# Performance work log

Hardware: AMD Instinct MI355X
Metric: run time of the kernel (lower is better)

The kernel has to match this reference:

```python
import jax, jax.numpy as jnp
import numpy as np

B, T, N, C_IN, C_OUT, D_E, GH, H = 16, 12, 2048, 64, 64, 16, 32, 4


def setup_inputs() -> dict:
    key = jax.random.key(0)
    ks = jax.random.split(key, 12)
    f = jax.random.normal
    return {
        "x": f(ks[0], (B, T, N, C_IN), jnp.float32),
        "init_state": jnp.zeros((B, N, C_OUT), jnp.float32),
        "node_embeddings": f(ks[1], (N, D_E), jnp.float32),
        "gat_W": f(ks[2], (H, D_E, GH), jnp.float32) * 0.3,
        "gat_a_src": f(ks[3], (H, GH), jnp.float32) * 0.3,
        "gat_a_dst": f(ks[4], (H, GH), jnp.float32) * 0.3,
        "wp_gates": f(ks[5], (D_E, 2, C_IN + C_OUT, 2 * C_OUT), jnp.float32) * 0.05,
        "bp_gates": f(ks[6], (D_E, 2 * C_OUT), jnp.float32) * 0.05,
        "wp_cand": f(ks[7], (D_E, 2, C_IN + C_OUT, C_OUT), jnp.float32) * 0.05,
        "bp_cand": f(ks[8], (D_E, C_OUT), jnp.float32) * 0.05,
        "tc_w": f(ks[9], (C_OUT, C_OUT, 1, 3), jnp.float32) * 0.05,
        "tc_b": jnp.zeros((C_OUT,), jnp.float32),
        "rc_w": f(ks[10], (C_OUT, C_IN, 1, 1), jnp.float32) * 0.05,
        "rc_b": jnp.zeros((C_OUT,), jnp.float32),
        "ln_g": jnp.ones((C_OUT,), jnp.float32),
        "ln_b": jnp.zeros((C_OUT,), jnp.float32),
    }


def _forward(x, init_state, node_embeddings, gat_W, gat_a_src, gat_a_dst,
             wp_gates, bp_gates, wp_cand, bp_cand, tc_w, tc_b, rc_w, rc_b, ln_g, ln_b):
    E = node_embeddings
    # GAT-style adaptive support over node embeddings: [N, N]
    h = jnp.einsum('nd,hdf->hnf', E, gat_W)                       # [H,N,GH]
    s = jnp.einsum('hnf,hf->hn', h, gat_a_src)
    d = jnp.einsum('hnf,hf->hn', h, gat_a_dst)
    e = jax.nn.leaky_relu(s[:, :, None] + d[:, None, :], 0.2)     # [H,N,N]
    A = jax.nn.softmax(e, axis=-1).mean(0)                        # [N,N]
    # node-adaptive weights (NAL): per-node weights from embedding pools
    W_g = jnp.einsum('nd,dkio->nkio', E, wp_gates)                # [N,2,Cin+Cout,2Cout]
    b_g = E @ bp_gates                                            # [N,2Cout]
    W_c = jnp.einsum('nd,dkio->nkio', E, wp_cand)
    b_c = E @ bp_cand

    def gconv(inp, W, b):
        # cheb order-2 supports [I, A] over inp: [B,N,C] -> [B,N,out]
        xg = jnp.stack([inp, jnp.einsum('mn,bnc->bmc', A, inp)], 2)
        return jnp.einsum('bnki,nkio->bno', xg, W) + b

    def step(state, xt):
        zr = jax.nn.sigmoid(gconv(jnp.concatenate([xt, state], -1), W_g, b_g))
        z, r = jnp.split(zr, 2, axis=-1)
        hc = jnp.tanh(gconv(jnp.concatenate([xt, r * state], -1), W_c, b_c))
        new = z * state + (1.0 - z) * hc
        return new, new

    last, inner = jax.lax.scan(step, init_state, jnp.swapaxes(x, 0, 1))
    inner = jnp.swapaxes(inner, 0, 1)                             # [B,T,N,C]

    cur = jnp.transpose(inner, (0, 3, 2, 1))                      # [B,C,N,T]
    tco = jax.lax.conv_general_dilated(
        cur, tc_w, (1, 1), [(0, 0), (1, 1)],
        dimension_numbers=('NCHW', 'OIHW', 'NCHW')) + tc_b[None, :, None, None]
    xp = jnp.transpose(x, (0, 3, 2, 1))                           # [B,Cin,N,T]
    res = jnp.einsum('oc,bcnt->bont', rc_w[:, :, 0, 0], xp) + rc_b[None, :, None, None]
    y = jnp.transpose(jax.nn.relu(res + tco), (0, 3, 2, 1))       # [B,T,N,C]
    mu = y.mean(-1, keepdims=True)
    var = y.var(-1, keepdims=True)
    y = (y - mu) / jnp.sqrt(var + 1e-5) * ln_g + ln_b
    return y, last


def reference(x, init_state, node_embeddings, gat_W, gat_a_src, gat_a_dst,
              wp_gates, bp_gates, wp_cand, bp_cand, tc_w, tc_b, rc_w, rc_b, ln_g, ln_b):
    y, last = _forward(x, init_state, node_embeddings, gat_W, gat_a_src, gat_a_dst,
                       wp_gates, bp_gates, wp_cand, bp_cand, tc_w, tc_b, rc_w, rc_b, ln_g, ln_b)
    return (y, last)
```

## Files before the change

### kernel.cpp

```cpp
#include <hip/hip_runtime.h>
#include <stdint.h>

#define B_  16
#define T_  12
#define N_  2048
#define DE_ 16
#define GH_ 32
#define NH_ 4

typedef __attribute__((ext_vector_type(8)))  short short8;
typedef __attribute__((ext_vector_type(4)))  float f32x4;
typedef __attribute__((ext_vector_type(16))) float f32x16;

__device__ __forceinline__ unsigned short f2b(float f){
  unsigned u = __float_as_uint(f);
  return (unsigned short)((u + 0x7fffu + ((u>>16)&1u)) >> 16);
}
__device__ __forceinline__ float b2f(unsigned short h){
  return __uint_as_float(((unsigned)h)<<16);
}
__device__ __forceinline__ unsigned pk2(float a, float b){
  return (unsigned)f2b(a) | ((unsigned)f2b(b)<<16);
}
__device__ __forceinline__ float lrelu(float v){ return v>=0.f ? v : 0.2f*v; }

__device__ __forceinline__ void gl16(const void* g, void* l){
  __builtin_amdgcn_global_load_lds((const __attribute__((address_space(1))) void*)g,
                                   (__attribute__((address_space(3))) void*)l, 16, 0, 0);
}

__global__ __launch_bounds__(256) void k_gat_sd(const float* __restrict__ E, const float* __restrict__ gW,
    const float* __restrict__ asrc, const float* __restrict__ adst,
    float* __restrict__ sArr, float* __restrict__ dArr)
{
  int id = blockIdx.x*256 + threadIdx.x;
  int h = id >> 11, n = id & 2047;
  float hv[GH_];
#pragma unroll
  for (int f=0; f<GH_; ++f) hv[f]=0.f;
  for (int d=0; d<DE_; ++d){
    float e = E[n*DE_+d];
    const float* wr = gW + (h*DE_+d)*GH_;
#pragma unroll
    for (int f=0; f<GH_; ++f) hv[f] += e*wr[f];
  }
  float s=0.f, dd=0.f;
#pragma unroll
  for (int f=0; f<GH_; ++f){ s += hv[f]*asrc[h*GH_+f]; dd += hv[f]*adst[h*GH_+f]; }
  sArr[h*N_+n]=s; dArr[h*N_+n]=dd;
}

__global__ __launch_bounds__(256) void k_dmax(const float* __restrict__ dArr, float* __restrict__ dmax){
  __shared__ float red[256];
  int h = blockIdx.x, t = threadIdx.x;
  float m = -1e30f;
  for (int i=t;i<N_;i+=256) m = fmaxf(m, dArr[h*N_+i]);
  red[t]=m; __syncthreads();
  for (int s=128;s>0;s>>=1){ if (t<s) red[t]=fmaxf(red[t],red[t+s]); __syncthreads(); }
  if (t==0) dmax[h]=red[0];
}

__global__ __launch_bounds__(256) void k_denom(const float* __restrict__ sArr, const float* __restrict__ dArr,
                                               const float* __restrict__ dmax, float* __restrict__ denom){
  __shared__ float red[256];
  int m = blockIdx.x, h = blockIdx.y, t = threadIdx.x;
  float sm = sArr[h*N_+m];
  float shift = lrelu(sm + dmax[h]);
  float acc=0.f;
  for (int i=t;i<N_;i+=256) acc += __expf(lrelu(sm + dArr[h*N_+i]) - shift);
  red[t]=acc; __syncthreads();
  for (int s=128;s>0;s>>=1){ if (t<s) red[t]+=red[t+s]; __syncthreads(); }
  if (t==0) denom[h*N_+m]=red[0];
}

__global__ __launch_bounds__(256) void k_adj(const float* __restrict__ sArr, const float* __restrict__ dArr,
                                             const float* __restrict__ dmax, const float* __restrict__ denom,
                                             unsigned short* __restrict__ Abf){
  int m = blockIdx.x, t = threadIdx.x;
  float sm[NH_], sh[NH_], inv[NH_];
#pragma unroll
  for (int h=0;h<NH_;++h){ sm[h]=sArr[h*N_+m]; sh[h]=lrelu(sm[h]+dmax[h]); inv[h]=1.f/denom[h*N_+m]; }
  for (int n=t;n<N_;n+=256){
    float acc=0.f;
#pragma unroll
    for (int h=0;h<NH_;++h) acc += __expf(lrelu(sm[h]+dArr[h*N_+n]) - sh[h]) * inv[h];
    Abf[(long)m*N_+n] = f2b(acc*0.25f);
  }
}

__global__ __launch_bounds__(256) void k_xsw(const float* __restrict__ x,
                                             unsigned short* __restrict__ xsw)
{
  __shared__ unsigned short sT[256*64];
  int kb = blockIdx.x;
  int btB = blockIdx.y;
  int tid = threadIdx.x;
  int btl = tid>>6, kin = tid&63;
  int n  = kb*64 + kin;
  int bt = btB*4 + btl;
  const float* src = x + ((long)bt*N_ + n)*64;
  unsigned short row[64];
#pragma unroll
  for (int c4=0; c4<16; ++c4){
    float4 v = *(const float4*)(src + c4*4);
    row[c4*4+0]=f2b(v.x); row[c4*4+1]=f2b(v.y); row[c4*4+2]=f2b(v.z); row[c4*4+3]=f2b(v.w);
  }
  int g0 = kin>>3, e = kin&7;
#pragma unroll
  for (int c=0; c<64; ++c){
    int jl = btl*64 + c;
    int s = g0 ^ (c&7);
    sT[jl*64 + s*8 + e] = row[c];
  }
  __syncthreads();
  unsigned short* dst = xsw + ((long)kb*12288 + btB*256)*64;
  const uint4* sp = (const uint4*)sT;
  uint4* dp = (uint4*)dst;
  for (int i=tid; i<2048; i+=256) dp[i] = sp[i];
}

__global__ __launch_bounds__(256) void k_nalw(const float* __restrict__ E, const float* __restrict__ wp,
                                              unsigned short* __restrict__ Wout, int Osz){
  __shared__ float sS[256][17];
  __shared__ float sE[512*16];
  int o = blockIdx.x, q = blockIdx.y, t = threadIdx.x;
  int slot = t>>3, j = t&7;
  int kio = (((slot ^ (o&7))&31)<<3) | j;
  long dstride = 256L*Osz;
  for (int d=0; d<DE_; ++d) sS[t][d] = wp[d*dstride + (long)kio*Osz + o];
  for (int i=t; i<512*16; i+=256) sE[i] = E[q*512*16 + i];
  __syncthreads();
  unsigned short* out = Wout + (long)(q*512)*dstride + o*256 + t;
  for (int nn=0; nn<512; ++nn){
    float acc=0.f;
    const float* e = &sE[nn*16];
#pragma unroll
    for (int d=0; d<DE_; ++d) acc += e[d]*sS[t][d];
    out[(long)nn*dstride] = f2b(acc);
  }
}

__global__ __launch_bounds__(256) void k_nalb(const float* __restrict__ E, const float* __restrict__ bpg,
                                              const float* __restrict__ bpc,
                                              unsigned short* __restrict__ bg, unsigned short* __restrict__ bc){
  int id = blockIdx.x*256+threadIdx.x;
  int n = id/192, oo = id%192;
  float acc=0.f;
  if (oo<128){
    for (int d=0;d<DE_;++d) acc += E[n*DE_+d]*bpg[d*128+oo];
    bg[n*128+oo]=f2b(acc);
  } else {
    int c=oo-128;
    for (int d=0;d<DE_;++d) acc += E[n*DE_+d]*bpc[d*64+c];
    bc[n*64+c]=f2b(acc);
  }
}

__global__ __launch_bounds__(256) void k_wcat(const float* __restrict__ tcw, const float* __restrict__ rcw,
                                              unsigned short* __restrict__ Wcat){
  int id = blockIdx.x*256+threadIdx.x;
  int o = id>>8, k = id&255;
  float v;
  if (k<192){ int dt=k>>6, c=k&63; v = tcw[(o*64+c)*3+dt]; }
  else v = rcw[o*64 + (k&63)];
  int pos = o*256 + ((((k>>3)&31) ^ (o&7))<<3) + (k&7);
  Wcat[pos] = f2b(v);
}

__global__ __launch_bounds__(256) void k_init2(const float* __restrict__ init, float* __restrict__ st,
                                               unsigned short* __restrict__ stb){
  int i = blockIdx.x*256+threadIdx.x;
  float v = init[i]; st[i]=v;
  int c = i&63, n = (i>>6)&2047, b = i>>17;
  int kb = n>>6, kin = n&63;
  int j = b*64 + c;
  int s = (kin>>3) ^ (c&7);
  stb[((long)kb*1024 + j)*64 + s*8 + (kin&7)] = f2b(v);
}

template<int BM, int BN, int JTOT>
__global__ __launch_bounds__(256) void k_gemm2(
    const unsigned short* __restrict__ A,
    const unsigned short* __restrict__ Bs,
    unsigned short* __restrict__ D)
{
  constexpr int MBLK = 2048/BM, MPX = MBLK/8;
  constexpr int NIA = BM*64*2/(256*16);
  constexpr int NIB = BN*64*2/(256*16);
  constexpr int WTM = BM/2, WTN = BN/2;
  constexpr int MTC = WTM/32, NTC = WTN/32;
  __shared__ __align__(16) unsigned short sA[BM*64];
  __shared__ __align__(16) unsigned short sB[BN*64];
  int bid = blockIdx.x;
  int xcd = bid & 7, idx = bid >> 3;
  int mB = xcd*MPX + (idx % MPX);
  int jB = idx / MPX;
  int tid = threadIdx.x, w = tid>>6, l = tid&63;
  int wm = w&1, wn = w>>1;
  f32x16 acc[MTC][NTC];
#pragma unroll
  for (int a=0;a<MTC;++a)
#pragma unroll
    for (int b=0;b<NTC;++b)
#pragma unroll
      for (int i=0;i<16;++i) acc[a][b][i]=0.f;

  for (int kb=0; kb<32; ++kb){
    __syncthreads();
#pragma unroll
    for (int i=0;i<NIA;++i){
      int c = (w*NIA+i)*64 + l;
      int row = c>>3, slot = c&7, g = slot ^ (row&7);
      gl16((const char*)A + (((long)(mB*BM+row))*2048 + kb*64 + g*8)*2,
           (char*)sA + (w*NIA+i)*1024);
    }
    const char* bt = (const char*)(Bs + ((long)kb*JTOT + jB*BN)*64);
#pragma unroll
    for (int i=0;i<NIB;++i)
      gl16(bt + ((w*NIB+i)*64 + l)*16, (char*)sB + (w*NIB+i)*1024);
    __syncthreads();
#pragma unroll
    for (int ks=0; ks<4; ++ks){
      int gk = ks*2 + (l>>5);
      short8 af[MTC];
#pragma unroll
      for (int mt=0; mt<MTC; ++mt){
        int row = wm*WTM + mt*32 + (l&31);
        af[mt] = *(const short8*)((const char*)sA + row*128 + ((gk ^ (row&7))<<4));
      }
#pragma unroll
      for (int nt=0; nt<NTC; ++nt){
        int jj = wn*WTN + nt*32 + (l&31);
        short8 bfv = *(const short8*)((const char*)sB + jj*128 + ((gk ^ (jj&7))<<4));
#pragma unroll
        for (int mt=0; mt<MTC; ++mt)
          acc[mt][nt] = __builtin_amdgcn_mfma_f32_32x32x16_bf16(af[mt], bfv, acc[mt][nt], 0,0,0);
      }
    }
  }
#pragma unroll
  for (int mt=0; mt<MTC; ++mt)
#pragma unroll
    for (int nt=0; nt<NTC; ++nt)
#pragma unroll
      for (int rg=0; rg<16; ++rg){
        int rl = wm*WTM + mt*32 + (rg&3) + 8*(rg>>2) + 4*(l>>5);
        int col = jB*BN + wn*WTN + nt*32 + (l&31);
        long m = (long)mB*BM + rl;
        D[m*JTOT + col] = f2b(acc[mt][nt][rg]);
      }
}

__global__ __launch_bounds__(256) void k_gates(
    const float* __restrict__ x, const float* __restrict__ st,
    const unsigned short* __restrict__ AXn, const unsigned short* __restrict__ AS,
    const unsigned short* __restrict__ Wg, const unsigned short* __restrict__ bg,
    float* __restrict__ zbuf, unsigned short* __restrict__ rsp,
    unsigned short* __restrict__ rsb, int t)
{
  __shared__ __align__(16) unsigned short sW[64*256];
  __shared__ __align__(16) unsigned short sX[16*256];
  int n = blockIdx.x, half = blockIdx.y;
  int tid = threadIdx.x, w = tid>>6, l = tid&63;
  const unsigned short* Wsrc = Wg + (long)n*32768 + half*16384;
#pragma unroll
  for (int i=0;i<8;++i){
    int c = (w*8+i)*64 + l;
    gl16((const char*)Wsrc + c*16, (char*)sW + (w*8+i)*1024);
  }
  int b = tid>>4, c16 = tid&15;
  uint4 g0, g1;
  if (c16 < 8){
    const float* p = (c16<4) ? (x  + (((long)(b*T_+t)*N_ + n)*64 + c16*16))
                             : (st + (((long)b*N_ + n)*64 + (c16-4)*16));
    float4 f0 = *(const float4*)(p+0), f1 = *(const float4*)(p+4);
    float4 f2v = *(const float4*)(p+8), f3 = *(const float4*)(p+12);
    g0.x = pk2(f0.x,f0.y); g0.y = pk2(f0.z,f0.w); g0.z = pk2(f1.x,f1.y); g0.w = pk2(f1.z,f1.w);
    g1.x = pk2(f2v.x,f2v.y); g1.y = pk2(f2v.z,f2v.w); g1.z = pk2(f3.x,f3.y); g1.w = pk2(f3.z,f3.w);
  } else {
    const unsigned short* p = (c16<12)
      ? (AXn + ((long)n*12288 + (b*T_+t)*64 + (c16-8)*16))
      : (AS  + ((long)n*1024  + b*64       + (c16-12)*16));
    g0 = *(const uint4*)(p); g1 = *(const uint4*)(p+8);
  }
  {
    int gg = c16*2;
    *(uint4*)((char*)sX + b*512 + (((gg  ) ^ (b&7))<<4)) = g0;
    *(uint4*)((char*)sX + b*512 + (((gg+1) ^ (b&7))<<4)) = g1;
  }
  __syncthreads();
  f32x4 acc;
#pragma unroll
  for (int i=0;i<4;++i) acc[i]=0.f;
  int orow = w*16 + (l&15);
  int arow = l&15;
#pragma unroll
  for (int ks=0; ks<8; ++ks){
    int g = ks*4 + (l>>4);
    short8 a = *(const short8*)((const char*)sX + arow*512 + ((g ^ (arow&7))<<4));
    short8 bb = *(const short8*)((const char*)sW + orow*512 + ((g ^ (orow&7))<<4));
    acc = __builtin_amdgcn_mfma_f32_16x16x32_bf16(a, bb, acc, 0,0,0);
  }
  int o = half*64 + orow;
  float bia = b2f(bg[n*128 + o]);
  int kb = n>>6, kin = n&63;
  int sw = (kin>>3) ^ (orow&7);
#pragma unroll
  for (int i=0;i<4;++i){
    int b2 = (l>>4)*4 + i;
    float v = acc[i] + bia;
    float sg = 1.f/(1.f+__expf(-v));
    long idx = ((long)b2*N_ + n)*64;
    if (half==0) zbuf[idx + o] = sg;
    else {
      float s0v = st[idx + orow];
      unsigned short rv = f2b(sg*s0v);
      rsp[idx + orow] = rv;
      rsb[((long)kb*1024 + b2*64 + orow)*64 + sw*8 + (kin&7)] = rv;
    }
  }
}

__global__ __launch_bounds__(256) void k_cand(
    const float* __restrict__ x, const float* __restrict__ zbuf,
    const unsigned short* __restrict__ AXn, const unsigned short* __restrict__ ARS,
    const unsigned short* __restrict__ rsp,
    const unsigned short* __restrict__ Wc, const unsigned short* __restrict__ bc,
    float* __restrict__ st, unsigned short* __restrict__ stb,
    unsigned short* __restrict__ inner, int t)
{
  __shared__ __align__(16) unsigned short sW[64*256];
  __shared__ __align__(16) unsigned short sX[16*256];
  int n = blockIdx.x;
  int tid = threadIdx.x, w = tid>>6, l = tid&63;
  const unsigned short* Wsrc = Wc + (long)n*16384;
#pragma unroll
  for (int i=0;i<8;++i){
    int c = (w*8+i)*64 + l;
    gl16((const char*)Wsrc + c*16, (char*)sW + (w*8+i)*1024);
  }
  int b = tid>>4, c16 = tid&15;
  uint4 g0, g1;
  if (c16 < 4){
    const float* p = x + (((long)(b*T_+t)*N_ + n)*64 + c16*16);
    float4 f0 = *(const float4*)(p+0), f1 = *(const float4*)(p+4);
    float4 f2v = *(const float4*)(p+8), f3 = *(const float4*)(p+12);
    g0.x = pk2(f0.x,f0.y); g0.y = pk2(f0.z,f0.w); g0.z = pk2(f1.x,f1.y); g0.w = pk2(f1.z,f1.w);
    g1.x = pk2(f2v.x,f2v.y); g1.y = pk2(f2v.z,f2v.w); g1.z = pk2(f3.x,f3.y); g1.w = pk2(f3.z,f3.w);
  } else {
    const unsigned short* p;
    if (c16<8)       p = rsp + (((long)b*N_ + n)*64 + (c16-4)*16);
    else if (c16<12) p = AXn + ((long)n*12288 + (b*T_+t)*64 + (c16-8)*16);
    else             p = ARS + ((long)n*1024  + b*64       + (c16-12)*16);
    g0 = *(const uint4*)(p); g1 = *(const uint4*)(p+8);
  }
  {
    int gg = c16*2;
    *(uint4*)((char*)sX + b*512 + (((gg  ) ^ (b&7))<<4)) = g0;
    *(uint4*)((char*)sX + b*512 + (((gg+1) ^ (b&7))<<4)) = g1;
  }
  __syncthreads();
  f32x4 acc;
#pragma unroll
  for (int i=0;i<4;++i) acc[i]=0.f;
  int orow = w*16 + (l&15);
  int arow = l&15;
#pragma unroll
  for (int ks=0; ks<8; ++ks){
    int g = ks*4 + (l>>4);
    short8 a = *(const short8*)((const char*)sX + arow*512 + ((g ^ (arow&7))<<4));
    short8 bb = *(const short8*)((const char*)sW + orow*512 + ((g ^ (orow&7))<<4));
    acc = __builtin_amdgcn_mfma_f32_16x16x32_bf16(a, bb, acc, 0,0,0);
  }
  float bia = b2f(bc[n*64 + orow]);
  int kb = n>>6, kin = n&63;
  int sw = (kin>>3) ^ (orow&7);
#pragma unroll
  for (int i=0;i<4;++i){
    int b2 = (l>>4)*4 + i;
    float hc = tanhf(acc[i] + bia);
    long idx = ((long)b2*N_ + n)*64 + orow;
    float zv = zbuf[idx];
    float olds = st[idx];
    float nv = zv*olds + (1.f-zv)*hc;
    st[idx]=nv;
    unsigned short nb = f2b(nv);
    stb[((long)kb*1024 + b2*64 + orow)*64 + sw*8 + (kin&7)] = nb;
    inner[((long)(b2*T_+t)*N_ + n)*64 + orow] = nb;
  }
}

__global__ __launch_bounds__(256) void k_post(
    const unsigned short* __restrict__ inner, const float* __restrict__ x,
    const unsigned short* __restrict__ Wcat,
    const float* __restrict__ tcb, const float* __restrict__ rcb,
    const float* __restrict__ lng, const float* __restrict__ lnb,
    float* __restrict__ out)
{
  __shared__ __align__(16) unsigned short sF[64*256];
  __shared__ __align__(16) unsigned short sW[64*256];
  int id = blockIdx.x;
  int bt = id>>5, nb = id&31;
  int b = bt/T_, t = bt%T_;
  int n0 = nb*64;
  int tid = threadIdx.x, w = tid>>6, l = tid&63;
#pragma unroll
  for (int i=0;i<8;++i){
    int c = (w*8+i)*64 + l;
    gl16((const char*)Wcat + c*16, (char*)sW + (w*8+i)*1024);
  }
  int row = tid&63, q = tid>>6;
  uint4 ch[8];
  if (q<3){
    int ts = t + q - 1;
    if (ts>=0 && ts<T_){
      const uint4* p = (const uint4*)(inner + (((long)(b*T_+ts)*N_) + n0+row)*64);
#pragma unroll
      for (int hh=0;hh<8;++hh) ch[hh]=p[hh];
    } else {
      uint4 zz; zz.x=0u; zz.y=0u; zz.z=0u; zz.w=0u;
#pragma unroll
      for (int hh=0;hh<8;++hh) ch[hh]=zz;
    }
  } else {
    const float4* p = (const float4*)(x + (((long)bt*N_) + n0+row)*64);
#pragma unroll
    for (int hh=0;hh<8;++hh){
      float4 u0=p[2*hh], u1=p[2*hh+1];
      ch[hh].x=pk2(u0.x,u0.y); ch[hh].y=pk2(u0.z,u0.w);
      ch[hh].z=pk2(u1.x,u1.y); ch[hh].w=pk2(u1.z,u1.w);
    }
  }
#pragma unroll
  for (int hh=0;hh<8;++hh){
    int g = q*8+hh;
    *(uint4*)((char*)sF + row*512 + ((g ^ (row&7))<<4)) = ch[hh];
  }
  __syncthreads();
  f32x4 acc[4];
#pragma unroll
  for (int ot=0; ot<4; ++ot)
#pragma unroll
    for (int i=0;i<4;++i) acc[ot][i]=0.f;
  int arow = w*16 + (l&15);
#pragma unroll
  for (int ks=0; ks<8; ++ks){
    int g = ks*4 + (l>>4);
    short8 a = *(const short8*)((const char*)sF + arow*512 + ((g ^ (arow&7))<<4));
#pragma unroll
    for (int ot=0; ot<4; ++ot){
      int o = ot*16 + (l&15);
      short8 bb = *(const short8*)((const char*)sW + o*512 + ((g ^ (o&7))<<4));
      acc[ot] = __builtin_amdgcn_mfma_f32_16x16x32_bf16(a, bb, acc[ot], 0,0,0);
    }
  }
  float s1[4]={0.f,0.f,0.f,0.f}, s2[4]={0.f,0.f,0.f,0.f};
#pragma unroll
  for (int ot=0; ot<4; ++ot){
    int o = ot*16 + (l&15);
    float bia = tcb[o] + rcb[o];
#pragma unroll
    for (int i=0;i<4;++i){
      float v = fmaxf(acc[ot][i] + bia, 0.f);
      acc[ot][i] = v;
      s1[i]+=v; s2[i]+=v*v;
    }
  }
#pragma unroll
  for (int msk=1; msk<16; msk<<=1){
#pragma unroll
    for (int i=0;i<4;++i){
      s1[i] += __shfl_xor(s1[i], msk, 64);
      s2[i] += __shfl_xor(s2[i], msk, 64);
    }
  }
#pragma unroll
  for (int i=0;i<4;++i){
    float mu = s1[i]*(1.f/64.f);
    float var = s2[i]*(1.f/64.f) - mu*mu;
    float rstd = rsqrtf(fmaxf(var,0.f)+1e-5f);
    int rr = n0 + w*16 + (l>>4)*4 + i;
#pragma unroll
    for (int ot=0; ot<4; ++ot){
      int o = ot*16 + (l&15);
      out[(((long)bt*N_) + rr)*64 + o] = (acc[ot][i]-mu)*rstd*lng[o] + lnb[o];
    }
  }
}

extern "C" void kernel_launch(void* const* d_in, const int* in_sizes, int n_in,
                              void* d_out, int out_size, void* d_ws, size_t ws_size,
                              hipStream_t stream)
{
  const float* x    = (const float*)d_in[0];
  const float* init = (const float*)d_in[1];
  const float* E    = (const float*)d_in[2];
  const float* gW   = (const float*)d_in[3];
  const float* asrc = (const float*)d_in[4];
  const float* adst = (const float*)d_in[5];
  const float* wpg  = (const float*)d_in[6];
  const float* bpg  = (const float*)d_in[7];
  const float* wpc  = (const float*)d_in[8];
  const float* bpc  = (const float*)d_in[9];
  const float* tcw  = (const float*)d_in[10];
  const float* tcb  = (const float*)d_in[11];
  const float* rcw  = (const float*)d_in[12];
  const float* rcb  = (const float*)d_in[13];
  const float* lng  = (const float*)d_in[14];
  const float* lnb  = (const float*)d_in[15];
  float* out = (float*)d_out;

  char* p = (char*)d_ws;
  auto alloc = [&](size_t bytes)->char*{ char* r = p; p += (bytes + 255) & ~(size_t)255; return r; };
  unsigned short* Abf  = (unsigned short*)alloc((size_t)N_*N_*2);
  unsigned short* Wg   = (unsigned short*)alloc((size_t)N_*32768*2);
  unsigned short* Wc   = (unsigned short*)alloc((size_t)N_*16384*2);
  unsigned short* bg   = (unsigned short*)alloc((size_t)N_*128*2);
  unsigned short* bc   = (unsigned short*)alloc((size_t)N_*64*2);
  unsigned short* xsw  = (unsigned short*)alloc((size_t)N_*12288*2);
  unsigned short* AXn  = (unsigned short*)alloc((size_t)N_*12288*2);
  unsigned short* AS   = (unsigned short*)alloc((size_t)N_*1024*2);
  unsigned short* ARS  = (unsigned short*)alloc((size_t)N_*1024*2);
  unsigned short* rsb  = (unsigned short*)alloc((size_t)N_*1024*2);
  unsigned short* rsp  = (unsigned short*)alloc((size_t)N_*1024*2);
  unsigned short* stb  = (unsigned short*)alloc((size_t)N_*1024*2);
  unsigned short* inner= (unsigned short*)alloc((size_t)B_*T_*N_*64*2);
  unsigned short* Wcat = (unsigned short*)alloc((size_t)64*256*2);
  float* sArr = (float*)alloc((size_t)NH_*N_*4);
  float* dArr = (float*)alloc((size_t)NH_*N_*4);
  float* dmax = (float*)alloc((size_t)NH_*4);
  float* denom= (float*)alloc((size_t)NH_*N_*4);
  float* stf  = (float*)alloc((size_t)B_*N_*64*4);
  float* zbuf = (float*)alloc((size_t)B_*N_*64*4);

  k_gat_sd<<<32,256,0,stream>>>(E,gW,asrc,adst,sArr,dArr);
  k_dmax<<<4,256,0,stream>>>(dArr,dmax);
  k_denom<<<dim3(N_,NH_),256,0,stream>>>(sArr,dArr,dmax,denom);
  k_adj<<<N_,256,0,stream>>>(sArr,dArr,dmax,denom,Abf);
  k_xsw<<<dim3(32,48),256,0,stream>>>(x,xsw);
  k_nalw<<<dim3(128,4),256,0,stream>>>(E,wpg,Wg,128);
  k_nalw<<<dim3(64,4),256,0,stream>>>(E,wpc,Wc,64);
  k_nalb<<<1536,256,0,stream>>>(E,bpg,bpc,bg,bc);
  k_wcat<<<64,256,0,stream>>>(tcw,rcw,Wcat);
  k_init2<<<(B_*N_*64)/256,256,0,stream>>>(init,stf,stb);

  k_gemm2<128,128,12288><<<1536,256,0,stream>>>(Abf, xsw, AXn);

  for (int t=0; t<T_; ++t){
    k_gemm2<64,64,1024><<<512,256,0,stream>>>(Abf, stb, AS);
    k_gates<<<dim3(N_,2),256,0,stream>>>(x,stf,AXn,AS,Wg,bg,zbuf,rsp,rsb,t);
    k_gemm2<64,64,1024><<<512,256,0,stream>>>(Abf, rsb, ARS);
    k_cand<<<N_,256,0,stream>>>(x,zbuf,AXn,ARS,rsp,Wc,bc,stf,stb,inner,t);
  }

  k_post<<<B_*T_*32,256,0,stream>>>(inner,x,Wcat,tcb,rcb,lng,lnb,out);
  hipMemcpyAsync(out + (size_t)B_*T_*N_*64, stf, (size_t)B_*N_*64*4,
                 hipMemcpyDeviceToDevice, stream);
}
```

Before: 2.102 ms.

## Precompute input-dependent gate/candidate terms for all timesteps before the recurrence

Splits the per-node weights into input (x, A·x) and state parts and computes the x-dependent contribution for all 12 timesteps in one batched MFMA kernel (k_pre) ahead of the scan. Inside the loop, the gates and candidate kernels then only load half the weights and do half the K dimension, adding the precomputed term from preA. The step loop also swaps the generic GEMM for a dedicated double-buffered 64x64 kernel with XCD-aware block mapping. This adds a large preA buffer (stored bf16, an extra rounding) and reuses workspace memory by aliasing buffers.

```diff
diff --git a/kernel.cpp b/kernel.cpp
--- a/kernel.cpp
+++ b/kernel.cpp
@@ -119,24 +119,30 @@
   for (int i=tid; i<2048; i+=256) dp[i] = sp[i];
 }
 
-__global__ __launch_bounds__(256) void k_nalw(const float* __restrict__ E, const float* __restrict__ wp,
-                                              unsigned short* __restrict__ Wout, int Osz){
-  __shared__ float sS[256][17];
+__global__ __launch_bounds__(256) void k_nalw2(const float* __restrict__ E, const float* __restrict__ src,
+                                               unsigned short* __restrict__ dst,
+                                               int Osrc, int kofs, int o_dst0, long strideN)
+{
   __shared__ float sE[512*16];
-  int o = blockIdx.x, q = blockIdx.y, t = threadIdx.x;
-  int slot = t>>3, j = t&7;
-  int kio = (((slot ^ (o&7))&31)<<3) | j;
-  long dstride = 256L*Osz;
-  for (int d=0; d<DE_; ++d) sS[t][d] = wp[d*dstride + (long)kio*Osz + o];
-  for (int i=t; i<512*16; i+=256) sE[i] = E[q*512*16 + i];
+  int or_ = blockIdx.x, q = blockIdx.y, t = threadIdx.x;
+  int pos = t & 127, nsub = t >> 7;
+  int s = pos >> 3, j = pos & 7;
+  int k = ((s ^ (or_&7)) << 3) | j;
+  int cheb = k >> 6, i = kofs + (k & 63);
+  float wreg[16];
+#pragma unroll
+  for (int d=0; d<DE_; ++d)
+    wreg[d] = src[(long)d*2*128*Osrc + (long)cheb*128*Osrc + (long)i*Osrc + or_];
+  for (int idx=t; idx<512*16; idx+=256) sE[idx] = E[q*512*16 + idx];
   __syncthreads();
-  unsigned short* out = Wout + (long)(q*512)*dstride + o*256 + t;
-  for (int nn=0; nn<512; ++nn){
+  unsigned short* out = dst + (long)(q*512)*strideN + (o_dst0 + or_)*128 + pos;
+  for (int nn=0; nn<256; ++nn){
+    int nl = nn*2 + nsub;
+    const float* e = &sE[nl*16];
     float acc=0.f;
-    const float* e = &sE[nn*16];
-#pragma unroll
-    for (int d=0; d<DE_; ++d) acc += e[d]*sS[t][d];
-    out[(long)nn*dstride] = f2b(acc);
+#pragma unroll
+    for (int d=0; d<DE_; ++d) acc += e[d]*wreg[d];
+    out[(long)nl*strideN] = f2b(acc);
   }
 }
 
@@ -251,43 +257,154 @@
       }
 }
 
-__global__ __launch_bounds__(256) void k_gates(
-    const float* __restrict__ x, const float* __restrict__ st,
-    const unsigned short* __restrict__ AXn, const unsigned short* __restrict__ AS,
-    const unsigned short* __restrict__ Wg, const unsigned short* __restrict__ bg,
+__global__ __launch_bounds__(256) void k_gemm_s(
+    const unsigned short* __restrict__ A,
+    const unsigned short* __restrict__ Bs,
+    unsigned short* __restrict__ D)
+{
+  __shared__ __align__(16) unsigned short sA[2][64*64];
+  __shared__ __align__(16) unsigned short sB[2][64*64];
+  int bid = blockIdx.x;
+  int xcd = bid & 7, idx = bid >> 3;
+  int mB = xcd*4 + (idx & 3);
+  int jB = idx >> 2;
+  int tid = threadIdx.x, w = tid>>6, l = tid&63;
+  int wm = w&1, wn = w>>1;
+  f32x16 acc;
+#pragma unroll
+  for (int i=0;i<16;++i) acc[i]=0.f;
+
+  auto stage = [&](int p, int kb){
+#pragma unroll
+    for (int i=0;i<2;++i){
+      int c = (w*2+i)*64 + l;
+      int row = c>>3, slot = c&7, g = slot ^ (row&7);
+      gl16((const char*)A + (((long)(mB*64+row))*2048 + kb*64 + g*8)*2,
+           (char*)sA[p] + (w*2+i)*1024);
+    }
+    const char* bt = (const char*)(Bs + ((long)kb*1024 + jB*64)*64);
+#pragma unroll
+    for (int i=0;i<2;++i)
+      gl16(bt + ((w*2+i)*64 + l)*16, (char*)sB[p] + (w*2+i)*1024);
+  };
+
+  stage(0, 0);
+  __syncthreads();
+  for (int kb=0; kb<32; ++kb){
+    int p = kb & 1;
+    if (kb < 31) stage(p^1, kb+1);
+#pragma unroll
+    for (int ks=0; ks<4; ++ks){
+      int gk = ks*2 + (l>>5);
+      int row = wm*32 + (l&31);
+      short8 af = *(const short8*)((const char*)sA[p] + row*128 + ((gk ^ (row&7))<<4));
+      int jj = wn*32 + (l&31);
+      short8 bfv = *(const short8*)((const char*)sB[p] + jj*128 + ((gk ^ (jj&7))<<4));
+      acc = __builtin_amdgcn_mfma_f32_32x32x16_bf16(af, bfv, acc, 0,0,0);
+    }
+    __syncthreads();
+  }
+#pragma unroll
+  for (int rg=0; rg<16; ++rg){
+    int rl = wm*32 + (rg&3) + 8*(rg>>2) + 4*(l>>5);
+    int col = jB*64 + wn*32 + (l&31);
+    long m = (long)mB*64 + rl;
+    D[m*1024 + col] = f2b(acc[rg]);
+  }
+}
+
+__global__ __launch_bounds__(256) void k_pre(
+    const float* __restrict__ x, const unsigned short* __restrict__ AXn,
+    const unsigned short* __restrict__ Wx, unsigned short* __restrict__ preA)
+{
+  __shared__ __align__(16) unsigned short sX[192*128];
+  __shared__ __align__(16) unsigned short sW[48*128];
+  int n = blockIdx.x;
+  int tid = threadIdx.x, w = tid>>6, l = tid&63;
+  int rsub = tid>>4, kg = tid&15;
+#pragma unroll
+  for (int i=0;i<12;++i){
+    int row = i*16 + rsub;
+    uint4 v;
+    if (kg<8){
+      const float* p = x + ((long)row*N_ + n)*64 + kg*8;
+      float4 a0 = *(const float4*)p, a1 = *(const float4*)(p+4);
+      v.x = pk2(a0.x,a0.y); v.y = pk2(a0.z,a0.w); v.z = pk2(a1.x,a1.y); v.w = pk2(a1.z,a1.w);
+    } else {
+      v = *(const uint4*)(AXn + (long)n*12288 + row*64 + (kg-8)*8);
+    }
+    *(uint4*)((char*)sX + row*256 + ((kg ^ (row&7))<<4)) = v;
+  }
+  const char* wsrc = (const char*)(Wx + (long)n*192*128);
+  for (int oc=0; oc<4; ++oc){
+    __syncthreads();
+#pragma unroll
+    for (int i=0;i<3;++i)
+      gl16(wsrc + oc*12288 + ((w*3+i)*64 + l)*16, (char*)sW + (w*3+i)*1024);
+    __syncthreads();
+    f32x4 acc[3][3];
+#pragma unroll
+    for (int mt=0;mt<3;++mt)
+#pragma unroll
+      for (int ot=0;ot<3;++ot)
+#pragma unroll
+        for (int i=0;i<4;++i) acc[mt][ot][i]=0.f;
+#pragma unroll
+    for (int ks=0; ks<4; ++ks){
+      int g = ks*4 + (l>>4);
+      short8 a[3];
+#pragma unroll
+      for (int mt=0;mt<3;++mt){
+        int row = w*48 + mt*16 + (l&15);
+        a[mt] = *(const short8*)((const char*)sX + row*256 + ((g ^ (row&7))<<4));
+      }
+#pragma unroll
+      for (int ot=0;ot<3;++ot){
+        int rb = ot*16 + (l&15);
+        short8 bb = *(const short8*)((const char*)sW + rb*256 + ((g ^ (rb&7))<<4));
+#pragma unroll
+        for (int mt=0;mt<3;++mt)
+          acc[mt][ot] = __builtin_amdgcn_mfma_f32_16x16x32_bf16(a[mt], bb, acc[mt][ot], 0,0,0);
+      }
+    }
+#pragma unroll
+    for (int mt=0;mt<3;++mt)
+#pragma unroll
+      for (int ot=0;ot<3;++ot)
+#pragma unroll
+        for (int i=0;i<4;++i){
+          int rl = w*48 + mt*16 + (l>>4)*4 + i;
+          int o = oc*48 + ot*16 + (l&15);
+          preA[((long)n*192 + rl)*192 + o] = f2b(acc[mt][ot][i]);
+        }
+  }
+}
+
+__global__ __launch_bounds__(256) void k_gates2(
+    const float* __restrict__ st, const unsigned short* __restrict__ AS,
+    const unsigned short* __restrict__ Wsg, const unsigned short* __restrict__ bg,
+    const unsigned short* __restrict__ preA,
     float* __restrict__ zbuf, unsigned short* __restrict__ rsp,
-    unsigned short* __restrict__ rsb, int t)
-{
-  __shared__ __align__(16) unsigned short sW[64*256];
-  __shared__ __align__(16) unsigned short sX[16*256];
+    unsigned short* __restrict__ rsb, int tstep)
+{
+  __shared__ __align__(16) unsigned short sW[64*128];
+  __shared__ __align__(16) unsigned short sX[16*128];
   int n = blockIdx.x, half = blockIdx.y;
   int tid = threadIdx.x, w = tid>>6, l = tid&63;
-  const unsigned short* Wsrc = Wg + (long)n*32768 + half*16384;
-#pragma unroll
-  for (int i=0;i<8;++i){
-    int c = (w*8+i)*64 + l;
-    gl16((const char*)Wsrc + c*16, (char*)sW + (w*8+i)*1024);
-  }
-  int b = tid>>4, c16 = tid&15;
-  uint4 g0, g1;
-  if (c16 < 8){
-    const float* p = (c16<4) ? (x  + (((long)(b*T_+t)*N_ + n)*64 + c16*16))
-                             : (st + (((long)b*N_ + n)*64 + (c16-4)*16));
-    float4 f0 = *(const float4*)(p+0), f1 = *(const float4*)(p+4);
-    float4 f2v = *(const float4*)(p+8), f3 = *(const float4*)(p+12);
-    g0.x = pk2(f0.x,f0.y); g0.y = pk2(f0.z,f0.w); g0.z = pk2(f1.x,f1.y); g0.w = pk2(f1.z,f1.w);
-    g1.x = pk2(f2v.x,f2v.y); g1.y = pk2(f2v.z,f2v.w); g1.z = pk2(f3.x,f3.y); g1.w = pk2(f3.z,f3.w);
+  const char* wsrc = (const char*)(Wsg + (long)n*16384 + half*8192);
+#pragma unroll
+  for (int i=0;i<4;++i)
+    gl16(wsrc + ((w*4+i)*64 + l)*16, (char*)sW + (w*4+i)*1024);
+  int b = tid>>4, kg = tid&15;
+  uint4 v;
+  if (kg<8){
+    const float* p = st + ((long)(b*N_ + n))*64 + kg*8;
+    float4 a0 = *(const float4*)p, a1 = *(const float4*)(p+4);
+    v.x = pk2(a0.x,a0.y); v.y = pk2(a0.z,a0.w); v.z = pk2(a1.x,a1.y); v.w = pk2(a1.z,a1.w);
   } else {
-    const unsigned short* p = (c16<12)
-      ? (AXn + ((long)n*12288 + (b*T_+t)*64 + (c16-8)*16))
-      : (AS  + ((long)n*1024  + b*64       + (c16-12)*16));
-    g0 = *(const uint4*)(p); g1 = *(const uint4*)(p+8);
-  }
-  {
-    int gg = c16*2;
-    *(uint4*)((char*)sX + b*512 + (((gg  ) ^ (b&7))<<4)) = g0;
-    *(uint4*)((char*)sX + b*512 + (((gg+1) ^ (b&7))<<4)) = g1;
-  }
+    v = *(const uint4*)(AS + (long)n*1024 + b*64 + (kg-8)*8);
+  }
+  *(uint4*)((char*)sX + b*256 + ((kg ^ (b&7))<<4)) = v;
   __syncthreads();
   f32x4 acc;
 #pragma unroll
@@ -295,10 +412,10 @@
   int orow = w*16 + (l&15);
   int arow = l&15;
 #pragma unroll
-  for (int ks=0; ks<8; ++ks){
+  for (int ks=0; ks<4; ++ks){
     int g = ks*4 + (l>>4);
-    short8 a = *(const short8*)((const char*)sX + arow*512 + ((g ^ (arow&7))<<4));
-    short8 bb = *(const short8*)((const char*)sW + orow*512 + ((g ^ (orow&7))<<4));
+    short8 a = *(const short8*)((const char*)sX + arow*256 + ((g ^ (arow&7))<<4));
+    short8 bb = *(const short8*)((const char*)sW + orow*256 + ((g ^ (orow&7))<<4));
     acc = __builtin_amdgcn_mfma_f32_16x16x32_bf16(a, bb, acc, 0,0,0);
   }
   int o = half*64 + orow;
@@ -308,8 +425,9 @@
 #pragma unroll
   for (int i=0;i<4;++i){
     int b2 = (l>>4)*4 + i;
-    float v = acc[i] + bia;
-    float sg = 1.f/(1.f+__expf(-v));
+    float pre = b2f(preA[((long)n*192 + b2*T_ + tstep)*192 + o]);
+    float vv = acc[i] + bia + pre;
+    float sg = 1.f/(1.f+__expf(-vv));
     long idx = ((long)b2*N_ + n)*64;
     if (half==0) zbuf[idx + o] = sg;
     else {
@@ -321,44 +439,27 @@
   }
 }
 
-__global__ __launch_bounds__(256) void k_cand(
-    const float* __restrict__ x, const float* __restrict__ zbuf,
-    const unsigned short* __restrict__ AXn, const unsigned short* __restrict__ ARS,
-    const unsigned short* __restrict__ rsp,
-    const unsigned short* __restrict__ Wc, const unsigned short* __restrict__ bc,
+__global__ __launch_bounds__(256) void k_cand2(
+    const float* __restrict__ zbuf,
+    const unsigned short* __restrict__ ARS, const unsigned short* __restrict__ rsp,
+    const unsigned short* __restrict__ Wsc, const unsigned short* __restrict__ bc,
+    const unsigned short* __restrict__ preA,
     float* __restrict__ st, unsigned short* __restrict__ stb,
-    unsigned short* __restrict__ inner, int t)
-{
-  __shared__ __align__(16) unsigned short sW[64*256];
-  __shared__ __align__(16) unsigned short sX[16*256];
+    unsigned short* __restrict__ inner, int tstep)
+{
+  __shared__ __align__(16) unsigned short sW[64*128];
+  __shared__ __align__(16) unsigned short sX[16*128];
   int n = blockIdx.x;
   int tid = threadIdx.x, w = tid>>6, l = tid&63;
-  const unsigned short* Wsrc = Wc + (long)n*16384;
-#pragma unroll
-  for (int i=0;i<8;++i){
-    int c = (w*8+i)*64 + l;
-    gl16((const char*)Wsrc + c*16, (char*)sW + (w*8+i)*1024);
-  }
-  int b = tid>>4, c16 = tid&15;
-  uint4 g0, g1;
-  if (c16 < 4){
-    const float* p = x + (((long)(b*T_+t)*N_ + n)*64 + c16*16);
-    float4 f0 = *(const float4*)(p+0), f1 = *(const float4*)(p+4);
-    float4 f2v = *(const float4*)(p+8), f3 = *(const float4*)(p+12);
-    g0.x = pk2(f0.x,f0.y); g0.y = pk2(f0.z,f0.w); g0.z = pk2(f1.x,f1.y); g0.w = pk2(f1.z,f1.w);
-    g1.x = pk2(f2v.x,f2v.y); g1.y = pk2(f2v.z,f2v.w); g1.z = pk2(f3.x,f3.y); g1.w = pk2(f3.z,f3.w);
-  } else {
-    const unsigned short* p;
-    if (c16<8)       p = rsp + (((long)b*N_ + n)*64 + (c16-4)*16);
-    else if (c16<12) p = AXn + ((long)n*12288 + (b*T_+t)*64 + (c16-8)*16);
-    else             p = ARS + ((long)n*1024  + b*64       + (c16-12)*16);
-    g0 = *(const uint4*)(p); g1 = *(const uint4*)(p+8);
-  }
-  {
-    int gg = c16*2;
-    *(uint4*)((char*)sX + b*512 + (((gg  ) ^ (b&7))<<4)) = g0;
-    *(uint4*)((char*)sX + b*512 + (((gg+1) ^ (b&7))<<4)) = g1;
-  }
+  const char* wsrc = (const char*)(Wsc + (long)n*8192);
+#pragma unroll
+  for (int i=0;i<4;++i)
+    gl16(wsrc + ((w*4+i)*64 + l)*16, (char*)sW + (w*4+i)*1024);
+  int b = tid>>4, kg = tid&15;
+  uint4 v;
+  if (kg<8) v = *(const uint4*)(rsp + ((long)(b*N_ + n))*64 + kg*8);
+  else      v = *(const uint4*)(ARS + (long)n*1024 + b*64 + (kg-8)*8);
+  *(uint4*)((char*)sX + b*256 + ((kg ^ (b&7))<<4)) = v;
   __syncthreads();
   f32x4 acc;
 #pragma unroll
@@ -366,10 +467,10 @@
   int orow = w*16 + (l&15);
   int arow = l&15;
 #pragma unroll
-  for (int ks=0; ks<8; ++ks){
+  for (int ks=0; ks<4; ++ks){
     int g = ks*4 + (l>>4);
-    short8 a = *(const short8*)((const char*)sX + arow*512 + ((g ^ (arow&7))<<4));
-    short8 bb = *(const short8*)((const char*)sW + orow*512 + ((g ^ (orow&7))<<4));
+    short8 a = *(const short8*)((const char*)sX + arow*256 + ((g ^ (arow&7))<<4));
+    short8 bb = *(const short8*)((const char*)sW + orow*256 + ((g ^ (orow&7))<<4));
     acc = __builtin_amdgcn_mfma_f32_16x16x32_bf16(a, bb, acc, 0,0,0);
   }
   float bia = b2f(bc[n*64 + orow]);
@@ -378,7 +479,8 @@
 #pragma unroll
   for (int i=0;i<4;++i){
     int b2 = (l>>4)*4 + i;
-    float hc = tanhf(acc[i] + bia);
+    float pre = b2f(preA[((long)n*192 + b2*T_ + tstep)*192 + 128 + orow]);
+    float hc = tanhf(acc[i] + bia + pre);
     long idx = ((long)b2*N_ + n)*64 + orow;
     float zv = zbuf[idx];
     float olds = st[idx];
@@ -386,7 +488,7 @@
     st[idx]=nv;
     unsigned short nb = f2b(nv);
     stb[((long)kb*1024 + b2*64 + orow)*64 + sw*8 + (kin&7)] = nb;
-    inner[((long)(b2*T_+t)*N_ + n)*64 + orow] = nb;
+    inner[((long)(b2*T_+tstep)*N_ + n)*64 + orow] = nb;
   }
 }
 
@@ -513,12 +615,15 @@
   char* p = (char*)d_ws;
   auto alloc = [&](size_t bytes)->char*{ char* r = p; p += (bytes + 255) & ~(size_t)255; return r; };
   unsigned short* Abf  = (unsigned short*)alloc((size_t)N_*N_*2);
-  unsigned short* Wg   = (unsigned short*)alloc((size_t)N_*32768*2);
-  unsigned short* Wc   = (unsigned short*)alloc((size_t)N_*16384*2);
+  unsigned short* WPool= (unsigned short*)alloc((size_t)N_*192*128*2);
+  unsigned short* Wx   = WPool;
+  unsigned short* Wsg  = WPool;
+  unsigned short* Wsc  = WPool + (size_t)N_*128*128;
+  unsigned short* preA = (unsigned short*)alloc((size_t)N_*192*192*2);
+  unsigned short* xsw  = preA;
+  unsigned short* AXn  = (unsigned short*)alloc((size_t)N_*12288*2);
   unsigned short* bg   = (unsigned short*)alloc((size_t)N_*128*2);
   unsigned short* bc   = (unsigned short*)alloc((size_t)N_*64*2);
-  unsigned short* xsw  = (unsigned short*)alloc((size_t)N_*12288*2);
-  unsigned short* AXn  = (unsigned short*)alloc((size_t)N_*12288*2);
   unsigned short* AS   = (unsigned short*)alloc((size_t)N_*1024*2);
   unsigned short* ARS  = (unsigned short*)alloc((size_t)N_*1024*2);
   unsigned short* rsb  = (unsigned short*)alloc((size_t)N_*1024*2);
@@ -538,19 +643,22 @@
   k_denom<<<dim3(N_,NH_),256,0,stream>>>(sArr,dArr,dmax,denom);
   k_adj<<<N_,256,0,stream>>>(sArr,dArr,dmax,denom,Abf);
   k_xsw<<<dim3(32,48),256,0,stream>>>(x,xsw);
-  k_nalw<<<dim3(128,4),256,0,stream>>>(E,wpg,Wg,128);
-  k_nalw<<<dim3(64,4),256,0,stream>>>(E,wpc,Wc,64);
+  k_nalw2<<<dim3(128,4),256,0,stream>>>(E,wpg,Wx, 128, 0,   0, 192L*128);
+  k_nalw2<<<dim3(64,4),256,0,stream>>>(E,wpc,Wx,  64, 0, 128, 192L*128);
   k_nalb<<<1536,256,0,stream>>>(E,bpg,bpc,bg,bc);
   k_wcat<<<64,256,0,stream>>>(tcw,rcw,Wcat);
   k_init2<<<(B_*N_*64)/256,256,0,stream>>>(init,stf,stb);
 
   k_gemm2<128,128,12288><<<1536,256,0,stream>>>(Abf, xsw, AXn);
+  k_pre<<<N_,256,0,stream>>>(x, AXn, Wx, preA);
+  k_nalw2<<<dim3(128,4),256,0,stream>>>(E,wpg,Wsg,128,64,   0, 128L*128);
+  k_nalw2<<<dim3(64,4),256,0,stream>>>(E,wpc,Wsc, 64,64,   0,  64L*128);
 
   for (int t=0; t<T_; ++t){
-    k_gemm2<64,64,1024><<<512,256,0,stream>>>(Abf, stb, AS);
-    k_gates<<<dim3(N_,2),256,0,stream>>>(x,stf,AXn,AS,Wg,bg,zbuf,rsp,rsb,t);
-    k_gemm2<64,64,1024><<<512,256,0,stream>>>(Abf, rsb, ARS);
-    k_cand<<<N_,256,0,stream>>>(x,zbuf,AXn,ARS,rsp,Wc,bc,stf,stb,inner,t);
+    k_gemm_s<<<512,256,0,stream>>>(Abf, stb, AS);
+    k_gates2<<<dim3(N_,2),256,0,stream>>>(stf,AS,Wsg,bg,preA,zbuf,rsp,rsb,t);
+    k_gemm_s<<<512,256,0,stream>>>(Abf, rsb, ARS);
+    k_cand2<<<N_,256,0,stream>>>(zbuf,ARS,rsp,Wsc,bc,preA,stf,stb,inner,t);
   }
 
   k_post<<<B_*T_*32,256,0,stream>>>(inner,x,Wcat,tcb,rcb,lng,lnb,out);
```

Measured after the change: 2.132 ms. About the same (+1.4%).
